# Optimization experiments

Measured on AMD Instinct MI355X. Metric: run time of the kernel, lower is better.

## Reference

```python
import jax, jax.numpy as jnp
import numpy as np

N = 100000      # nodes
DEG = 32        # padded max neighbors
C_IN = 128
C_OUT = 128


def setup_inputs() -> dict:
    key = jax.random.key(0)
    k1, k2, k3 = jax.random.split(key, 3)
    x = jax.random.normal(k1, (N, C_IN), dtype=jnp.float32)
    # neighbor indices in [0, N]; index N points at the appended zero padding row
    edge_index = jax.random.randint(k2, (N, DEG), 0, N + 1, dtype=jnp.int64)
    eps = jnp.zeros((1,), dtype=jnp.float32)
    W = jax.random.normal(k3, (C_OUT, C_IN), dtype=jnp.float32) * (1.0 / np.sqrt(C_IN))
    b = jnp.zeros((C_OUT,), dtype=jnp.float32)
    return {"x": x, "edge_index": edge_index, "eps": eps, "W": W, "b": b}


def reference(x, edge_index, eps, W, b):
    # pad with a zero row so index N gathers zeros (padding neighbors)
    padded = jnp.concatenate([x, jnp.zeros((1, x.shape[1]), dtype=x.dtype)], axis=0)  # [N+1, C]
    neigh = padded[edge_index]              # [N, DEG, C] gather
    agg = neigh.sum(axis=1)                 # [N, C] sum-aggregate
    h = (1.0 + eps) * x + agg               # scale self + add neighbors
    return h @ W.T + b                      # Linear: [N, C_OUT]
```

## Files before the change

### kernel.cpp

```cpp
#include <hip/hip_runtime.h>
#include <stdint.h>

#define NN 100000
#define DEG 32
#define CC 128
#define SW 136
#define SIDW 36
#define QMAX 6.0f

typedef __attribute__((ext_vector_type(4))) float f32x4;
typedef __attribute__((ext_vector_type(4))) unsigned int u32x4;
typedef __attribute__((ext_vector_type(8))) short s16x8;

static __device__ __forceinline__ unsigned short f2b(float f) {
    unsigned u = __float_as_uint(f);
    u += 0x7fffu + ((u >> 16) & 1u);
    return (unsigned short)(u >> 16);
}

__global__ __launch_bounds__(256) void cvt_xq(const float* __restrict__ x,
                                              unsigned int* __restrict__ xq) {
    const float qsi = 127.0f / QMAX;
    int i = blockIdx.x * blockDim.x + threadIdx.x;
    const int total = (NN + 1) * CC / 16;
    const int nx = NN * CC / 16;
    for (; i < total; i += gridDim.x * blockDim.x) {
        u32x4 o = {0x80808080u, 0x80808080u, 0x80808080u, 0x80808080u};
        if (i < nx) {
            const f32x4* p = (const f32x4*)(x + (size_t)i * 16);
            #pragma unroll
            for (int q = 0; q < 4; ++q) {
                f32x4 v = p[q];
                unsigned d = 0;
                #pragma unroll
                for (int j = 0; j < 4; ++j) {
                    float t = fminf(fmaxf(v[j] * qsi, -127.0f), 127.0f);
                    int qi = (int)rintf(t) + 128;
                    d |= ((unsigned)qi & 0xffu) << (8 * j);
                }
                o[q] = d;
            }
        }
        ((u32x4*)xq)[i] = o;
    }
}

__global__ __launch_bounds__(256) void cvt_w(const float* __restrict__ W,
                                             unsigned short* __restrict__ Wb) {
    int i = blockIdx.x * 256 + threadIdx.x;
    f32x4 v = ((const f32x4*)W)[i];
    ushort4 o;
    o.x = f2b(v[0]); o.y = f2b(v[1]); o.z = f2b(v[2]); o.w = f2b(v[3]);
    ((ushort4*)Wb)[i] = o;
}

__global__ __launch_bounds__(128) void gin_i8(
    const unsigned char* __restrict__ xq, const int* __restrict__ ei,
    const float* __restrict__ eps_p, const unsigned short* __restrict__ Wb,
    const float* __restrict__ bias, float* __restrict__ out) {
    __shared__ int sid[2][16 * SIDW];
    __shared__ unsigned short sA[2][16 * SW];

    const int tid = threadIdx.x;
    const int w = tid >> 6, l = tid & 63;
    const int wbase = blockIdx.x * 32 + w * 16;

    {
        const int r = l >> 2;
        const int row = wbase + r;
        const int j0 = (l & 3) * 8;
        int4 a, b;
        if (row < NN) {
            const int4* p = (const int4*)(ei + (size_t)row * DEG + j0);
            a = p[0]; b = p[1];
        } else {
            a.x = NN; a.y = NN; a.z = NN; a.w = NN; b = a;
        }
        int* dst = sid[w] + r * SIDW + j0;
        *(int4*)dst = a;
        *(int4*)(dst + 4) = b;
    }

    const float qs = QMAX / 127.0f;
    const float es2 = (1.0f + eps_p[0]) * qs;
    const float c0 = qs * 4096.0f + es2 * 128.0f;

    const int rr = l >> 3;
    const int c4 = l & 7;
    const unsigned char* bx = xq + c4 * 16;

    #pragma unroll
    for (int g = 0; g < 2; ++g) {
        const int rloc = g * 8 + rr;
        const int* idp = sid[w] + rloc * SIDW;

        unsigned accL[4], accH[4];
        #pragma unroll
        for (int q = 0; q < 4; ++q) { accL[q] = 0u; accH[q] = 0u; }

        u32x4 gbuf[2][8];
        {
            int4 i0 = *(const int4*)(idp);
            int4 i1 = *(const int4*)(idp + 4);
            gbuf[0][0] = *(const u32x4*)(bx + (size_t)i0.x * CC);
            gbuf[0][1] = *(const u32x4*)(bx + (size_t)i0.y * CC);
            gbuf[0][2] = *(const u32x4*)(bx + (size_t)i0.z * CC);
            gbuf[0][3] = *(const u32x4*)(bx + (size_t)i0.w * CC);
            gbuf[0][4] = *(const u32x4*)(bx + (size_t)i1.x * CC);
            gbuf[0][5] = *(const u32x4*)(bx + (size_t)i1.y * CC);
            gbuf[0][6] = *(const u32x4*)(bx + (size_t)i1.z * CC);
            gbuf[0][7] = *(const u32x4*)(bx + (size_t)i1.w * CC);
        }
        #pragma unroll
        for (int tc = 0; tc < 4; ++tc) {
            if (tc < 3) {
                int4 i0 = *(const int4*)(idp + (tc + 1) * 8);
                int4 i1 = *(const int4*)(idp + (tc + 1) * 8 + 4);
                const int nb = (tc + 1) & 1;
                gbuf[nb][0] = *(const u32x4*)(bx + (size_t)i0.x * CC);
                gbuf[nb][1] = *(const u32x4*)(bx + (size_t)i0.y * CC);
                gbuf[nb][2] = *(const u32x4*)(bx + (size_t)i0.z * CC);
                gbuf[nb][3] = *(const u32x4*)(bx + (size_t)i0.w * CC);
                gbuf[nb][4] = *(const u32x4*)(bx + (size_t)i1.x * CC);
                gbuf[nb][5] = *(const u32x4*)(bx + (size_t)i1.y * CC);
                gbuf[nb][6] = *(const u32x4*)(bx + (size_t)i1.z * CC);
                gbuf[nb][7] = *(const u32x4*)(bx + (size_t)i1.w * CC);
            }
            #pragma unroll
            for (int t = 0; t < 8; ++t) {
                u32x4 v = gbuf[tc & 1][t];
                #pragma unroll
                for (int q = 0; q < 4; ++q) {
                    unsigned d = v[q];
                    accL[q] += d & 0x00ff00ffu;
                    accH[q] += (d >> 8) & 0x00ff00ffu;
                }
            }
        }

        const int row = wbase + rloc;
        const int srow = (row < NN) ? row : NN;
        u32x4 sv = *(const u32x4*)(xq + (size_t)srow * CC + c4 * 16);
        unsigned short hb[16];
        #pragma unroll
        for (int q = 0; q < 4; ++q) {
            unsigned d = sv[q];
            float s0 = (float)(d & 0xffu);
            float s1 = (float)((d >> 8) & 0xffu);
            float s2 = (float)((d >> 16) & 0xffu);
            float s3 = (float)(d >> 24);
            float a0 = (float)(accL[q] & 0xffffu);
            float a2 = (float)(accL[q] >> 16);
            float a1 = (float)(accH[q] & 0xffffu);
            float a3 = (float)(accH[q] >> 16);
            hb[q * 4 + 0] = f2b(fmaf(qs, a0, fmaf(es2, s0, -c0)));
            hb[q * 4 + 1] = f2b(fmaf(qs, a1, fmaf(es2, s1, -c0)));
            hb[q * 4 + 2] = f2b(fmaf(qs, a2, fmaf(es2, s2, -c0)));
            hb[q * 4 + 3] = f2b(fmaf(qs, a3, fmaf(es2, s3, -c0)));
        }
        unsigned short* ap = sA[w] + rloc * SW + c4 * 16;
        s16x8 o0, o1;
        #pragma unroll
        for (int j = 0; j < 8; ++j) { o0[j] = (short)hb[j]; o1[j] = (short)hb[8 + j]; }
        *(s16x8*)ap = o0;
        *(s16x8*)(ap + 8) = o1;
    }

    const int c = l & 15, s = l >> 4;
    s16x8 afrag[4];
    #pragma unroll
    for (int kt = 0; kt < 4; ++kt)
        afrag[kt] = *(const s16x8*)(sA[w] + c * SW + kt * 32 + s * 8);

    f32x4 acc[8];
    #pragma unroll
    for (int nt = 0; nt < 8; ++nt) acc[nt] = (f32x4){0.f, 0.f, 0.f, 0.f};
    #pragma unroll
    for (int nt = 0; nt < 8; ++nt) {
        #pragma unroll
        for (int kt = 0; kt < 4; ++kt) {
            s16x8 bfrag = *(const s16x8*)(Wb + (size_t)(nt * 16 + c) * CC + kt * 32 + s * 8);
            acc[nt] = __builtin_amdgcn_mfma_f32_16x16x32_bf16(afrag[kt], bfrag, acc[nt], 0, 0, 0);
        }
    }

    #pragma unroll
    for (int nt = 0; nt < 8; ++nt) {
        const float bv = bias[nt * 16 + c];
        #pragma unroll
        for (int j = 0; j < 4; ++j) {
            const int orow = wbase + s * 4 + j;
            if (orow < NN) out[(size_t)orow * CC + nt * 16 + c] = acc[nt][j] + bv;
        }
    }
}

__global__ __launch_bounds__(256) void gin_f32(
    const float* __restrict__ x, const int* __restrict__ ei,
    const float* __restrict__ eps_p, const float* __restrict__ W,
    const float* __restrict__ bias, float* __restrict__ out) {
    __shared__ int sidx[DEG][64 + 2];
    const int tid = threadIdx.x;
    const int base = blockIdx.x * 64;
    for (int q = tid; q < 64 * DEG; q += 256) {
        int r = q >> 5, d = q & 31;
        int row = base + r;
        sidx[d][r] = (row < NN) ? ei[row * DEG + d] : NN;
    }
    __syncthreads();
    const int w = tid >> 6, l = tid & 63;
    const int lr = l & 15, lk = l >> 4;
    const int kb = lk * 8;
    const int rloc = w * 16 + lr;
    const int arow = base + rloc;
    const float eps1 = 1.0f + eps_p[0];
    float hacc[4][8];
    {
        int sr = (arow < NN) ? arow : 0;
        #pragma unroll
        for (int kt = 0; kt < 4; ++kt) {
            const f32x4* p = (const f32x4*)(x + (size_t)sr * CC + kt * 32 + kb);
            f32x4 a = p[0], b = p[1];
            #pragma unroll
            for (int j = 0; j < 4; ++j) { hacc[kt][j] = eps1 * a[j]; hacc[kt][4 + j] = eps1 * b[j]; }
        }
    }
    #pragma unroll 4
    for (int d = 0; d < DEG; ++d) {
        int id = sidx[d][rloc];
        if (id < NN) {
            const float* gp = x + (size_t)id * CC + kb;
            #pragma unroll
            for (int kt = 0; kt < 4; ++kt) {
                f32x4 a = *(const f32x4*)(gp + kt * 32);
                f32x4 b = *(const f32x4*)(gp + kt * 32 + 4);
                #pragma unroll
                for (int j = 0; j < 4; ++j) { hacc[kt][j] += a[j]; hacc[kt][4 + j] += b[j]; }
            }
        }
    }
    s16x8 afrag[4];
    #pragma unroll
    for (int kt = 0; kt < 4; ++kt)
        #pragma unroll
        for (int j = 0; j < 8; ++j) afrag[kt][j] = (short)f2b(hacc[kt][j]);
    f32x4 acc[8];
    #pragma unroll
    for (int nt = 0; nt < 8; ++nt) acc[nt] = (f32x4){0.f, 0.f, 0.f, 0.f};
    #pragma unroll
    for (int nt = 0; nt < 8; ++nt) {
        #pragma unroll
        for (int kt = 0; kt < 4; ++kt) {
            s16x8 bfrag;
            const f32x4* p = (const f32x4*)(W + (size_t)(nt * 16 + lr) * CC + kt * 32 + kb);
            f32x4 a = p[0], b = p[1];
            #pragma unroll
            for (int j = 0; j < 4; ++j) { bfrag[j] = (short)f2b(a[j]); bfrag[4 + j] = (short)f2b(b[j]); }
            acc[nt] = __builtin_amdgcn_mfma_f32_16x16x32_bf16(afrag[kt], bfrag, acc[nt], 0, 0, 0);
        }
    }
    #pragma unroll
    for (int nt = 0; nt < 8; ++nt) {
        float bv = bias[nt * 16 + lr];
        #pragma unroll
        for (int j = 0; j < 4; ++j) {
            int orow = base + w * 16 + lk * 4 + j;
            if (orow < NN) out[(size_t)orow * CC + nt * 16 + lr] = acc[nt][j] + bv;
        }
    }
}

extern "C" void kernel_launch(void* const* d_in, const int* in_sizes, int n_in,
                              void* d_out, int out_size, void* d_ws, size_t ws_size,
                              hipStream_t stream) {
    const float* x = (const float*)d_in[0];
    const int* ei = (const int*)d_in[1];
    const float* eps = (const float*)d_in[2];
    const float* W = (const float*)d_in[3];
    const float* b = (const float*)d_in[4];
    float* out = (float*)d_out;

    const size_t xq_bytes = (size_t)(NN + 1) * CC;
    const size_t need = xq_bytes + (size_t)CC * CC * sizeof(unsigned short);
    const int grid = (NN + 31) / 32;

    if (ws_size >= need) {
        unsigned char* xqp = (unsigned char*)d_ws;
        unsigned short* Wbp = (unsigned short*)(xqp + xq_bytes);
        cvt_xq<<<2048, 256, 0, stream>>>(x, (unsigned int*)xqp);
        cvt_w<<<16, 256, 0, stream>>>(W, Wbp);
        gin_i8<<<grid, 128, 0, stream>>>(xqp, ei, eps, Wbp, b, out);
    } else {
        gin_f32<<<(NN + 63) / 64, 256, 0, stream>>>(x, ei, eps, W, b, out);
    }
}
```

Baseline: 87.75 us.

## Sort neighbor ids per row and gather in global index phases for locality

```diff
diff --git a/kernel.cpp b/kernel.cpp
--- a/kernel.cpp
+++ b/kernel.cpp
@@ -7,6 +7,8 @@
 #define SW 136
 #define SIDW 36
 #define QMAX 6.0f
+#define NPH 8
+#define PW 12501
 
 typedef __attribute__((ext_vector_type(4))) float f32x4;
 typedef __attribute__((ext_vector_type(4))) unsigned int u32x4;
@@ -54,10 +56,53 @@
     ((ushort4*)Wb)[i] = o;
 }
 
-__global__ __launch_bounds__(128) void gin_i8(
-    const unsigned char* __restrict__ xq, const int* __restrict__ ei,
-    const float* __restrict__ eps_p, const unsigned short* __restrict__ Wb,
-    const float* __restrict__ bias, float* __restrict__ out) {
+__global__ __launch_bounds__(256) void sort_ids(const int* __restrict__ ei,
+                                                int* __restrict__ sids,
+                                                unsigned long long* __restrict__ cnts) {
+    int row = blockIdx.x * 256 + threadIdx.x;
+    if (row >= NN) return;
+    int a[32];
+    const int4* p = (const int4*)(ei + (size_t)row * DEG);
+    #pragma unroll
+    for (int i = 0; i < 8; ++i) {
+        int4 v = p[i];
+        a[i * 4 + 0] = v.x; a[i * 4 + 1] = v.y; a[i * 4 + 2] = v.z; a[i * 4 + 3] = v.w;
+    }
+    #pragma unroll
+    for (int r = 0; r < 32; ++r) {
+        #pragma unroll
+        for (int i = (r & 1); i + 1 < 32; i += 2) {
+            int lo = a[i] < a[i + 1] ? a[i] : a[i + 1];
+            int hi = a[i] < a[i + 1] ? a[i + 1] : a[i];
+            a[i] = lo; a[i + 1] = hi;
+        }
+    }
+    unsigned long long packed = 0;
+    int prev = 0;
+    #pragma unroll
+    for (int k = 0; k < NPH; ++k) {
+        int bound = (k + 1) * PW;
+        int pos = 0;
+        #pragma unroll
+        for (int i = 0; i < 32; ++i) pos += (a[i] < bound) ? 1 : 0;
+        packed |= (unsigned long long)(unsigned)(pos - prev) << (8 * k);
+        prev = pos;
+    }
+    int4* q = (int4*)(sids + (size_t)row * DEG);
+    #pragma unroll
+    for (int i = 0; i < 8; ++i) {
+        int4 v;
+        v.x = a[i * 4 + 0]; v.y = a[i * 4 + 1]; v.z = a[i * 4 + 2]; v.w = a[i * 4 + 3];
+        q[i] = v;
+    }
+    cnts[row] = packed;
+}
+
+__global__ __launch_bounds__(128, 4) void gin_ph(
+    const unsigned char* __restrict__ xq, const int* __restrict__ sids,
+    const unsigned long long* __restrict__ cnts, const float* __restrict__ eps_p,
+    const unsigned short* __restrict__ Wb, const float* __restrict__ bias,
+    float* __restrict__ out) {
     __shared__ int sid[2][16 * SIDW];
     __shared__ unsigned short sA[2][16 * SW];
 
@@ -69,78 +114,87 @@
         const int r = l >> 2;
         const int row = wbase + r;
         const int j0 = (l & 3) * 8;
-        int4 a, b;
-        if (row < NN) {
-            const int4* p = (const int4*)(ei + (size_t)row * DEG + j0);
-            a = p[0]; b = p[1];
-        } else {
-            a.x = NN; a.y = NN; a.z = NN; a.w = NN; b = a;
-        }
+        const int4* p = (const int4*)(sids + (size_t)row * DEG + j0);
+        int4 a = p[0], b = p[1];
         int* dst = sid[w] + r * SIDW + j0;
         *(int4*)dst = a;
         *(int4*)(dst + 4) = b;
     }
-
-    const float qs = QMAX / 127.0f;
-    const float es2 = (1.0f + eps_p[0]) * qs;
-    const float c0 = qs * 4096.0f + es2 * 128.0f;
+    __syncthreads();
 
     const int rr = l >> 3;
     const int c4 = l & 7;
     const unsigned char* bx = xq + c4 * 16;
 
+    const unsigned long long c640 = cnts[wbase + rr];
+    const unsigned long long c641 = cnts[wbase + 8 + rr];
+    const unsigned cl0 = (unsigned)c640, ch0 = (unsigned)(c640 >> 32);
+    const unsigned cl1 = (unsigned)c641, ch1 = (unsigned)(c641 >> 32);
+
+    unsigned accL0[4] = {0, 0, 0, 0}, accH0[4] = {0, 0, 0, 0};
+    unsigned accL1[4] = {0, 0, 0, 0}, accH1[4] = {0, 0, 0, 0};
+    int p0 = 0, p1 = 0, T0 = 0, T1 = 0;
+
+#define ISS(dst, tt) { int pos_ = p + (tt); pos_ = pos_ < 31 ? pos_ : 31;        \
+    int id_ = sp[pos_];                                                          \
+    unsigned off_ = (unsigned)((((tt) < cnt) ? id_ : NN) * CC);                  \
+    dst = *(const u32x4*)(bx + off_); }
+#define CON(s) { accL[0] += s[0] & 0x00ff00ffu; accH[0] += (s[0] >> 8) & 0x00ff00ffu; \
+    accL[1] += s[1] & 0x00ff00ffu; accH[1] += (s[1] >> 8) & 0x00ff00ffu;              \
+    accL[2] += s[2] & 0x00ff00ffu; accH[2] += (s[2] >> 8) & 0x00ff00ffu;              \
+    accL[3] += s[3] & 0x00ff00ffu; accH[3] += (s[3] >> 8) & 0x00ff00ffu; }
+
+    auto run_group = [&](const int* sp, int p, const int cnt,
+                         unsigned (&accL)[4], unsigned (&accH)[4], int& T) {
+        int m = cnt;
+        { int t_ = __shfl_xor(m, 8);  m = m > t_ ? m : t_; }
+        { int t_ = __shfl_xor(m, 16); m = m > t_ ? m : t_; }
+        { int t_ = __shfl_xor(m, 32); m = m > t_ ? m : t_; }
+        const int nmax = __builtin_amdgcn_readfirstlane(m);
+        if (nmax <= 0) return;
+        u32x4 gA0, gA1, gA2, gA3, gB0, gB1, gB2, gB3;
+        ISS(gA0, 0) ISS(gA1, 1) ISS(gA2, 2) ISS(gA3, 3)
+        ISS(gB0, 4) ISS(gB1, 5) ISS(gB2, 6) ISS(gB3, 7)
+        int tb = 0;
+        for (;;) {
+            CON(gA0) CON(gA1) CON(gA2) CON(gA3)
+            T += 4; tb += 4;
+            if (tb >= nmax) break;
+            ISS(gA0, tb + 4) ISS(gA1, tb + 5) ISS(gA2, tb + 6) ISS(gA3, tb + 7)
+            CON(gB0) CON(gB1) CON(gB2) CON(gB3)
+            T += 4; tb += 4;
+            if (tb >= nmax) break;
+            ISS(gB0, tb + 4) ISS(gB1, tb + 5) ISS(gB2, tb + 6) ISS(gB3, tb + 7)
+        }
+    };
+
+    const int* sp0 = sid[w] + rr * SIDW;
+    const int* sp1 = sid[w] + (8 + rr) * SIDW;
+
+    #pragma unroll
+    for (int k = 0; k < NPH; ++k) {
+        const int cnt0 = (int)(((k < 4) ? (cl0 >> (8 * k)) : (ch0 >> (8 * (k - 4)))) & 0xffu);
+        const int cnt1 = (int)(((k < 4) ? (cl1 >> (8 * k)) : (ch1 >> (8 * (k - 4)))) & 0xffu);
+        run_group(sp0, p0, cnt0, accL0, accH0, T0);
+        p0 += cnt0;
+        run_group(sp1, p1, cnt1, accL1, accH1, T1);
+        p1 += cnt1;
+    }
+#undef ISS
+#undef CON
+
+    const float qs = QMAX / 127.0f;
+    const float es2 = (1.0f + eps_p[0]) * qs;
+
     #pragma unroll
     for (int g = 0; g < 2; ++g) {
+        const unsigned* aL = g ? accL1 : accL0;
+        const unsigned* aH = g ? accH1 : accH0;
+        const float Tf = 128.0f * (float)(g ? T1 : T0);
+        const float c0 = qs * Tf + es2 * 128.0f;
         const int rloc = g * 8 + rr;
-        const int* idp = sid[w] + rloc * SIDW;
-
-        unsigned accL[4], accH[4];
-        #pragma unroll
-        for (int q = 0; q < 4; ++q) { accL[q] = 0u; accH[q] = 0u; }
-
-        u32x4 gbuf[2][8];
-        {
-            int4 i0 = *(const int4*)(idp);
-            int4 i1 = *(const int4*)(idp + 4);
-            gbuf[0][0] = *(const u32x4*)(bx + (size_t)i0.x * CC);
-            gbuf[0][1] = *(const u32x4*)(bx + (size_t)i0.y * CC);
-            gbuf[0][2] = *(const u32x4*)(bx + (size_t)i0.z * CC);
-            gbuf[0][3] = *(const u32x4*)(bx + (size_t)i0.w * CC);
-            gbuf[0][4] = *(const u32x4*)(bx + (size_t)i1.x * CC);
-            gbuf[0][5] = *(const u32x4*)(bx + (size_t)i1.y * CC);
-            gbuf[0][6] = *(const u32x4*)(bx + (size_t)i1.z * CC);
-            gbuf[0][7] = *(const u32x4*)(bx + (size_t)i1.w * CC);
-        }
-        #pragma unroll
-        for (int tc = 0; tc < 4; ++tc) {
-            if (tc < 3) {
-                int4 i0 = *(const int4*)(idp + (tc + 1) * 8);
-                int4 i1 = *(const int4*)(idp + (tc + 1) * 8 + 4);
-                const int nb = (tc + 1) & 1;
-                gbuf[nb][0] = *(const u32x4*)(bx + (size_t)i0.x * CC);
-                gbuf[nb][1] = *(const u32x4*)(bx + (size_t)i0.y * CC);
-                gbuf[nb][2] = *(const u32x4*)(bx + (size_t)i0.z * CC);
-                gbuf[nb][3] = *(const u32x4*)(bx + (size_t)i0.w * CC);
-                gbuf[nb][4] = *(const u32x4*)(bx + (size_t)i1.x * CC);
-                gbuf[nb][5] = *(const u32x4*)(bx + (size_t)i1.y * CC);
-                gbuf[nb][6] = *(const u32x4*)(bx + (size_t)i1.z * CC);
-                gbuf[nb][7] = *(const u32x4*)(bx + (size_t)i1.w * CC);
-            }
-            #pragma unroll
-            for (int t = 0; t < 8; ++t) {
-                u32x4 v = gbuf[tc & 1][t];
-                #pragma unroll
-                for (int q = 0; q < 4; ++q) {
-                    unsigned d = v[q];
-                    accL[q] += d & 0x00ff00ffu;
-                    accH[q] += (d >> 8) & 0x00ff00ffu;
-                }
-            }
-        }
-
         const int row = wbase + rloc;
-        const int srow = (row < NN) ? row : NN;
-        u32x4 sv = *(const u32x4*)(xq + (size_t)srow * CC + c4 * 16);
+        u32x4 sv = *(const u32x4*)(xq + (size_t)row * CC + c4 * 16);
         unsigned short hb[16];
         #pragma unroll
         for (int q = 0; q < 4; ++q) {
@@ -149,10 +203,10 @@
             float s1 = (float)((d >> 8) & 0xffu);
             float s2 = (float)((d >> 16) & 0xffu);
             float s3 = (float)(d >> 24);
-            float a0 = (float)(accL[q] & 0xffffu);
-            float a2 = (float)(accL[q] >> 16);
-            float a1 = (float)(accH[q] & 0xffffu);
-            float a3 = (float)(accH[q] >> 16);
+            float a0 = (float)(aL[q] & 0xffffu);
+            float a2 = (float)(aL[q] >> 16);
+            float a1 = (float)(aH[q] & 0xffffu);
+            float a3 = (float)(aH[q] >> 16);
             hb[q * 4 + 0] = f2b(fmaf(qs, a0, fmaf(es2, s0, -c0)));
             hb[q * 4 + 1] = f2b(fmaf(qs, a1, fmaf(es2, s1, -c0)));
             hb[q * 4 + 2] = f2b(fmaf(qs, a2, fmaf(es2, s2, -c0)));
@@ -165,6 +219,7 @@
         *(s16x8*)ap = o0;
         *(s16x8*)(ap + 8) = o1;
     }
+    __syncthreads();
 
     const int c = l & 15, s = l >> 4;
     s16x8 afrag[4];
@@ -190,7 +245,7 @@
         #pragma unroll
         for (int j = 0; j < 4; ++j) {
             const int orow = wbase + s * 4 + j;
-            if (orow < NN) out[(size_t)orow * CC + nt * 16 + c] = acc[nt][j] + bv;
+            out[(size_t)orow * CC + nt * 16 + c] = acc[nt][j] + bv;
         }
     }
 }
@@ -281,15 +336,20 @@
     float* out = (float*)d_out;
 
     const size_t xq_bytes = (size_t)(NN + 1) * CC;
-    const size_t need = xq_bytes + (size_t)CC * CC * sizeof(unsigned short);
-    const int grid = (NN + 31) / 32;
+    const size_t wb_bytes = (size_t)CC * CC * sizeof(unsigned short);
+    const size_t sid_bytes = (size_t)NN * DEG * sizeof(int);
+    const size_t cnt_bytes = (size_t)NN * sizeof(unsigned long long);
+    const size_t need = xq_bytes + wb_bytes + sid_bytes + cnt_bytes;
 
     if (ws_size >= need) {
         unsigned char* xqp = (unsigned char*)d_ws;
         unsigned short* Wbp = (unsigned short*)(xqp + xq_bytes);
+        int* sidsp = (int*)(xqp + xq_bytes + wb_bytes);
+        unsigned long long* cntsp = (unsigned long long*)(xqp + xq_bytes + wb_bytes + sid_bytes);
         cvt_xq<<<2048, 256, 0, stream>>>(x, (unsigned int*)xqp);
         cvt_w<<<16, 256, 0, stream>>>(W, Wbp);
-        gin_i8<<<grid, 128, 0, stream>>>(xqp, ei, eps, Wbp, b, out);
+        sort_ids<<<(NN + 255) / 256, 256, 0, stream>>>(ei, sidsp, cntsp);
+        gin_ph<<<(NN + 31) / 32, 128, 0, stream>>>(xqp, sidsp, cntsp, eps, Wbp, b, out);
     } else {
         gin_f32<<<(NN + 63) / 64, 256, 0, stream>>>(x, ei, eps, W, b, out);
     }
```

Measured after the change: 102.3 us. 1.17x slower.
